# Performance work log

Hardware: AMD Instinct MI355X
Metric: run time of the kernel (lower is better)

The kernel has to match this reference:

```python
import jax, jax.numpy as jnp
import numpy as np

H = 5  # hidden size == input size

def setup_inputs() -> dict:
    key = jax.random.key(0)
    ks = jax.random.split(key, 12)
    B, T = 8192, 512
    s = 1.0 / np.sqrt(H)
    x = jax.random.normal(ks[0], (B, T, H), dtype=jnp.float32)
    # LSTM params (PyTorch layout: [4H, in], gate order i,f,g,o)
    W_ih = jax.random.uniform(ks[1], (4 * H, H), jnp.float32, -s, s)
    W_hh = jax.random.uniform(ks[2], (4 * H, H), jnp.float32, -s, s)
    b_ih = jax.random.uniform(ks[3], (4 * H,), jnp.float32, -s, s)
    b_hh = jax.random.uniform(ks[4], (4 * H,), jnp.float32, -s, s)
    # MLP head 5->32->32->5 (PyTorch Linear layout: [out, in])
    W1 = jax.random.uniform(ks[5], (32, H), jnp.float32, -s, s)
    b1 = jax.random.uniform(ks[6], (32,), jnp.float32, -s, s)
    s2 = 1.0 / np.sqrt(32)
    W2 = jax.random.uniform(ks[7], (32, 32), jnp.float32, -s2, s2)
    b2 = jax.random.uniform(ks[8], (32,), jnp.float32, -s2, s2)
    W3 = jax.random.uniform(ks[9], (H, 32), jnp.float32, -s2, s2)
    b3 = jax.random.uniform(ks[10], (H,), jnp.float32, -s2, s2)
    return {"x": x, "W_ih": W_ih, "W_hh": W_hh, "b_ih": b_ih, "b_hh": b_hh,
            "W1": W1, "b1": b1, "W2": W2, "b2": b2, "W3": W3, "b3": b3}


def _lstm_last_hidden(x, W_ih, W_hh, b_ih, b_hh):
    # x: [B, T, H]. Precompute input projections for all steps: [T, B, 4H]
    xz = jnp.einsum('bth,gh->tbg', x, W_ih) + (b_ih + b_hh)
    B = x.shape[0]
    h0 = jnp.zeros((B, H), x.dtype)
    c0 = jnp.zeros((B, H), x.dtype)

    def step(carry, z_t):
        h, c = carry
        z = z_t + h @ W_hh.T  # [B, 4H]
        i = jax.nn.sigmoid(z[:, 0:H])
        f = jax.nn.sigmoid(z[:, H:2 * H])
        g = jnp.tanh(z[:, 2 * H:3 * H])
        o = jax.nn.sigmoid(z[:, 3 * H:4 * H])
        c = f * c + i * g
        h = o * jnp.tanh(c)
        return (h, c), None

    (h, _), _ = jax.lax.scan(step, (h0, c0), xz)
    return h  # [B, H]


def reference(x, W_ih, W_hh, b_ih, b_hh, W1, b1, W2, b2, W3, b3):
    h_last = _lstm_last_hidden(x, W_ih, W_hh, b_ih, b_hh)
    out = h_last + x[:, -1, :]                # residual with last input step
    out = jax.nn.relu(out @ W1.T + b1)
    out = jax.nn.relu(out @ W2.T + b2)
    out = out @ W3.T + b3
    return out
```

## Files before the change

kernel.cpp:

```cpp
#include <hip/hip_runtime.h>


#define LOG2E 1.44269504088896f

__device__ __forceinline__ float hexp2(float x) { return __builtin_amdgcn_exp2f(x); }
__device__ __forceinline__ float hrcp(float x)  { return __builtin_amdgcn_rcpf(x); }

template<int CTRL>
__device__ __forceinline__ float dpp_mov(float x) {
  int r = __builtin_amdgcn_update_dpp(0, __builtin_bit_cast(int, x),
                                      CTRL, 0xF, 0xF, true);
  return __builtin_bit_cast(float, r);
}
template<int CTRL, int BANKMASK>
__device__ __forceinline__ float dpp_merge(float old, float src) {
  int r = __builtin_amdgcn_update_dpp(__builtin_bit_cast(int, old),
                                      __builtin_bit_cast(int, src),
                                      CTRL, 0xF, BANKMASK, false);
  return __builtin_bit_cast(float, r);
}

constexpr int TT   = 512;
constexpr int HD   = 5;
constexpr int RPB  = 8;
constexpr int CHNK = 32;
constexpr int RSTR = 164;
constexpr int XOFF = RPB * RSTR;
constexpr int NCH  = TT / CHNK;

__global__ __attribute__((amdgpu_flat_work_group_size(64, 64),
                          amdgpu_waves_per_eu(1, 1)))
void lstm_mlp_kernel(
    const float* __restrict__ x,   const float* __restrict__ Wih,
    const float* __restrict__ Whh, const float* __restrict__ bih,
    const float* __restrict__ bhh, const float* __restrict__ W1,
    const float* __restrict__ b1,  const float* __restrict__ W2,
    const float* __restrict__ b2,  const float* __restrict__ W3,
    const float* __restrict__ b3,  float* __restrict__ out, int B)
{
  const int lane = threadIdx.x;
  const int grp  = lane >> 3;
  const int j    = lane & 7;
  const int jj   = (j < 5) ? j : 0;
  const int blockRow = blockIdx.x * RPB;
  const int row  = blockRow + grp;
  const bool act = (j < 5) && (row < B);

  __shared__ __align__(16) float xbuf[2 * XOFF];
  __shared__ float s1[RPB][32];
  __shared__ float s2[RPB][32];

  float wih[4][5], whh[4][5], bsum[4];
#pragma unroll
  for (int G = 0; G < 4; ++G) {
    const float sc = (G == 2) ? (2.0f * LOG2E) : (-LOG2E);
#pragma unroll
    for (int k = 0; k < 5; ++k) {
      wih[G][k] = Wih[(G * 5 + jj) * 5 + k] * sc;
      whh[G][k] = Whh[(G * 5 + jj) * 5 + k] * sc;
    }
    bsum[G] = (bih[G * 5 + jj] + bhh[G * 5 + jj]) * sc;
  }

  const int rowc = (row < B) ? row : (B - 1);
  const float xl0 = x[(size_t)rowc * (TT * HD) + 511 * HD + 0];
  const float xl1 = x[(size_t)rowc * (TT * HD) + 511 * HD + 1];
  const float xl2 = x[(size_t)rowc * (TT * HD) + 511 * HD + 2];
  const float xl3 = x[(size_t)rowc * (TT * HD) + 511 * HD + 3];
  const float xl4 = x[(size_t)rowc * (TT * HD) + 511 * HD + 4];

  const float4* gp[5];
  int wa[5];
#pragma unroll
  for (int i = 0; i < 5; ++i) {
    int u  = i * 64 + lane;
    int r  = u / 40;
    int o4 = u - r * 40;
    int gr = blockRow + r; if (gr >= B) gr = B - 1;
    gp[i]  = (const float4*)(x + (size_t)gr * (TT * HD)) + o4;
    wa[i]  = r * RSTR + o4 * 4;
  }

  float4 st0, st1, st2, st3, st4;
  st0 = *gp[0]; gp[0] += 40; st1 = *gp[1]; gp[1] += 40;
  st2 = *gp[2]; gp[2] += 40; st3 = *gp[3]; gp[3] += 40;
  st4 = *gp[4]; gp[4] += 40;
  *(float4*)&xbuf[wa[0]] = st0; *(float4*)&xbuf[wa[1]] = st1;
  *(float4*)&xbuf[wa[2]] = st2; *(float4*)&xbuf[wa[3]] = st3;
  *(float4*)&xbuf[wa[4]] = st4;
  st0 = *gp[0]; gp[0] += 40; st1 = *gp[1]; gp[1] += 40;
  st2 = *gp[2]; gp[2] += 40; st3 = *gp[3]; gp[3] += 40;
  st4 = *gp[4]; gp[4] += 40;

  float c = 0.0f;
  float hv0 = 0.f, hv1 = 0.f, hv2 = 0.f, hv3 = 0.f, hv4 = 0.f;
  float zx0, zx1, zx2, zx3;

  {
    const float* xp = &xbuf[grp * RSTR];
    float p0 = xp[0], p1 = xp[1], p2 = xp[2], p3 = xp[3], p4 = xp[4];
    zx0 = bsum[0];
    zx0 = fmaf(p0, wih[0][0], zx0); zx0 = fmaf(p1, wih[0][1], zx0);
    zx0 = fmaf(p2, wih[0][2], zx0); zx0 = fmaf(p3, wih[0][3], zx0);
    zx0 = fmaf(p4, wih[0][4], zx0);
    zx1 = bsum[1];
    zx1 = fmaf(p0, wih[1][0], zx1); zx1 = fmaf(p1, wih[1][1], zx1);
    zx1 = fmaf(p2, wih[1][2], zx1); zx1 = fmaf(p3, wih[1][3], zx1);
    zx1 = fmaf(p4, wih[1][4], zx1);
    zx2 = bsum[2];
    zx2 = fmaf(p0, wih[2][0], zx2); zx2 = fmaf(p1, wih[2][1], zx2);
    zx2 = fmaf(p2, wih[2][2], zx2); zx2 = fmaf(p3, wih[2][3], zx2);
    zx2 = fmaf(p4, wih[2][4], zx2);
    zx3 = bsum[3];
    zx3 = fmaf(p0, wih[3][0], zx3); zx3 = fmaf(p1, wih[3][1], zx3);
    zx3 = fmaf(p2, wih[3][2], zx3); zx3 = fmaf(p3, wih[3][3], zx3);
    zx3 = fmaf(p4, wih[3][4], zx3);
  }

  auto stepP = [&](float n0, float n1, float n2, float n3, float n4) {
    float z0 = zx0, z1 = zx1, z2 = zx2, z3 = zx3;
    z0 = fmaf(hv0, whh[0][0], z0); z0 = fmaf(hv1, whh[0][1], z0);
    z0 = fmaf(hv2, whh[0][2], z0); z0 = fmaf(hv3, whh[0][3], z0);
    z0 = fmaf(hv4, whh[0][4], z0);
    z1 = fmaf(hv0, whh[1][0], z1); z1 = fmaf(hv1, whh[1][1], z1);
    z1 = fmaf(hv2, whh[1][2], z1); z1 = fmaf(hv3, whh[1][3], z1);
    z1 = fmaf(hv4, whh[1][4], z1);
    z2 = fmaf(hv0, whh[2][0], z2); z2 = fmaf(hv1, whh[2][1], z2);
    z2 = fmaf(hv2, whh[2][2], z2); z2 = fmaf(hv3, whh[2][3], z2);
    z2 = fmaf(hv4, whh[2][4], z2);
    z3 = fmaf(hv0, whh[3][0], z3); z3 = fmaf(hv1, whh[3][1], z3);
    z3 = fmaf(hv2, whh[3][2], z3); z3 = fmaf(hv3, whh[3][3], z3);
    z3 = fmaf(hv4, whh[3][4], z3);
    float e0 = hexp2(z0), e1 = hexp2(z1), e2 = hexp2(z2), e3 = hexp2(z3);
    float n_0 = bsum[0];
    n_0 = fmaf(n0, wih[0][0], n_0); n_0 = fmaf(n1, wih[0][1], n_0);
    n_0 = fmaf(n2, wih[0][2], n_0); n_0 = fmaf(n3, wih[0][3], n_0);
    n_0 = fmaf(n4, wih[0][4], n_0);
    float n_1 = bsum[1];
    n_1 = fmaf(n0, wih[1][0], n_1); n_1 = fmaf(n1, wih[1][1], n_1);
    n_1 = fmaf(n2, wih[1][2], n_1); n_1 = fmaf(n3, wih[1][3], n_1);
    n_1 = fmaf(n4, wih[1][4], n_1);
    float fg = hrcp(1.0f + e1);
    float ig = hrcp(1.0f + e0);
    float gr = hrcp(1.0f + e2);
    float og = hrcp(1.0f + e3);
    float gv = fmaf(-2.0f, gr, 1.0f);
    c = fmaf(fg, c, ig * gv);
    float cm = c * (2.0f * LOG2E);
    float ec = hexp2(cm);
    float n_2 = bsum[2];
    n_2 = fmaf(n0, wih[2][0], n_2); n_2 = fmaf(n1, wih[2][1], n_2);
    n_2 = fmaf(n2, wih[2][2], n_2); n_2 = fmaf(n3, wih[2][3], n_2);
    n_2 = fmaf(n4, wih[2][4], n_2);
    float n_3 = bsum[3];
    n_3 = fmaf(n0, wih[3][0], n_3); n_3 = fmaf(n1, wih[3][1], n_3);
    n_3 = fmaf(n2, wih[3][2], n_3); n_3 = fmaf(n3, wih[3][3], n_3);
    n_3 = fmaf(n4, wih[3][4], n_3);
    float th = fmaf(-2.0f, hrcp(1.0f + ec), 1.0f);
    float h  = og * th;
    float q0 = dpp_mov<0x00>(h);
    float q1 = dpp_mov<0x55>(h);
    float q2 = dpp_mov<0xAA>(h);
    float q3 = dpp_mov<0xFF>(h);
    hv0 = dpp_merge<0x114, 0xA>(q0, q0);
    hv1 = dpp_merge<0x114, 0xA>(q1, q1);
    hv2 = dpp_merge<0x114, 0xA>(q2, q2);
    hv3 = dpp_merge<0x114, 0xA>(q3, q3);
    hv4 = dpp_merge<0x104, 0x5>(q0, q0);
    zx0 = n_0; zx1 = n_1; zx2 = n_2; zx3 = n_3;
  };

  float4 A0, A1, A2, A3, A4;
  float4 B0, B1, B2, B3, B4;

  auto rdg = [&](int fi, float4& A, float4& Bv, float4& C, float4& D, float4& E) {
    const float4* p = (const float4*)&xbuf[fi];
    A = p[0]; Bv = p[1]; C = p[2]; D = p[3]; E = p[4];
  };

  auto SUBA = [&]() {
    stepP(A1.y, A1.z, A1.w, A2.x, A2.y);
    stepP(A2.z, A2.w, A3.x, A3.y, A3.z);
    stepP(A3.w, A4.x, A4.y, A4.z, A4.w);
    stepP(B0.x, B0.y, B0.z, B0.w, B1.x);
  };
  auto SUBB = [&]() {
    stepP(B1.y, B1.z, B1.w, B2.x, B2.y);
    stepP(B2.z, B2.w, B3.x, B3.y, B3.z);
    stepP(B3.w, B4.x, B4.y, B4.z, B4.w);
    stepP(A0.x, A0.y, A0.z, A0.w, A1.x);
  };

#pragma unroll 1
  for (int ch = 0; ch < NCH; ++ch) {
    const int bo_cur  = (ch & 1) ? XOFF : 0;
    const int bo_next = XOFF - bo_cur;
    if (ch < NCH - 1) {
      *(float4*)&xbuf[wa[0] + bo_next] = st0;
      *(float4*)&xbuf[wa[1] + bo_next] = st1;
      *(float4*)&xbuf[wa[2] + bo_next] = st2;
      *(float4*)&xbuf[wa[3] + bo_next] = st3;
      *(float4*)&xbuf[wa[4] + bo_next] = st4;
    }
    if (ch < NCH - 2) {
      st0 = *gp[0]; gp[0] += 40; st1 = *gp[1]; gp[1] += 40;
      st2 = *gp[2]; gp[2] += 40; st3 = *gp[3]; gp[3] += 40;
      st4 = *gp[4]; gp[4] += 40;
    }
    const int xb = bo_cur + grp * RSTR;
    rdg(xb +   0, A0, A1, A2, A3, A4);
    rdg(xb +  20, B0, B1, B2, B3, B4);
    SUBA(); rdg(xb +  40, A0, A1, A2, A3, A4);
    SUBB(); rdg(xb +  60, B0, B1, B2, B3, B4);
    SUBA(); rdg(xb +  80, A0, A1, A2, A3, A4);
    SUBB(); rdg(xb + 100, B0, B1, B2, B3, B4);
    SUBA(); rdg(xb + 120, A0, A1, A2, A3, A4);
    SUBB(); rdg(xb + 140, B0, B1, B2, B3, B4);
    SUBA();
    rdg(bo_next + grp * RSTR, A0, A1, A2, A3, A4);
    SUBB();
  }

  float in5_0 = hv0 + xl0, in5_1 = hv1 + xl1, in5_2 = hv2 + xl2,
        in5_3 = hv3 + xl3, in5_4 = hv4 + xl4;

#pragma unroll
  for (int p = 0; p < 4; ++p) {
    int m = p * 8 + j;
    float acc = b1[m];
    acc = fmaf(W1[m * 5 + 0], in5_0, acc);
    acc = fmaf(W1[m * 5 + 1], in5_1, acc);
    acc = fmaf(W1[m * 5 + 2], in5_2, acc);
    acc = fmaf(W1[m * 5 + 3], in5_3, acc);
    acc = fmaf(W1[m * 5 + 4], in5_4, acc);
    s1[grp][m] = fmaxf(acc, 0.0f);
  }
  float y1[32];
#pragma unroll
  for (int k = 0; k < 32; ++k) y1[k] = s1[grp][k];

  auto dot32 = [&](const float* W, int m, const float* y, float b) {
    float acc = b;
    const float4* w4 = (const float4*)(W + m * 32);
#pragma unroll
    for (int k4 = 0; k4 < 8; ++k4) {
      float4 w = w4[k4];
      acc = fmaf(w.x, y[k4 * 4 + 0], acc);
      acc = fmaf(w.y, y[k4 * 4 + 1], acc);
      acc = fmaf(w.z, y[k4 * 4 + 2], acc);
      acc = fmaf(w.w, y[k4 * 4 + 3], acc);
    }
    return acc;
  };

#pragma unroll
  for (int p = 0; p < 4; ++p) {
    int m = p * 8 + j;
    s2[grp][m] = fmaxf(dot32(W2, m, y1, b2[m]), 0.0f);
  }
  float y2[32];
#pragma unroll
  for (int k = 0; k < 32; ++k) y2[k] = s2[grp][k];

  if (act) out[row * HD + j] = dot32(W3, j, y2, b3[j]);
}

extern "C" void kernel_launch(void* const* d_in, const int* in_sizes, int n_in,
                              void* d_out, int out_size, void* d_ws, size_t ws_size,
                              hipStream_t stream) {
  const float* x   = (const float*)d_in[0];
  const float* Wih = (const float*)d_in[1];
  const float* Whh = (const float*)d_in[2];
  const float* bih = (const float*)d_in[3];
  const float* bhh = (const float*)d_in[4];
  const float* W1  = (const float*)d_in[5];
  const float* b1  = (const float*)d_in[6];
  const float* W2  = (const float*)d_in[7];
  const float* b2  = (const float*)d_in[8];
  const float* W3  = (const float*)d_in[9];
  const float* b3  = (const float*)d_in[10];

  int B = in_sizes[0] / (TT * HD);
  int grid = (B + RPB - 1) / RPB;
  hipLaunchKernelGGL(lstm_mlp_kernel, dim3(grid), dim3(64), 0, stream,
                     x, Wih, Whh, bih, bhh, W1, b1, W2, b2, W3, b3,
                     (float*)d_out, B);
}
```

Measured before the change: 204.5 us.

## Pair gate reciprocals, prefetch input projection two steps ahead, pin schedule

Gate reciprocals are combined in pairs: one rcp of (1+e0)(1+e2) and one of (1+e1)(1+e3) replace four separate rcps, and the gates are recovered with multiplies. This shortens the transcendental chain on the serial recurrence. The input projection is now computed two timesteps ahead, so the stepping offsets into the staged x buffer shift. sched_barrier calls pin how the off-critical-path projection FMAs interleave with the recurrence. The paired products can overflow if the gate exponents get large, and the gate exponent signs now rely on weights folded in elsewhere.

```diff
diff --git a/kernel.cpp b/kernel.cpp
--- a/kernel.cpp
+++ b/kernel.cpp
@@ -5,6 +5,7 @@
 
 __device__ __forceinline__ float hexp2(float x) { return __builtin_amdgcn_exp2f(x); }
 __device__ __forceinline__ float hrcp(float x)  { return __builtin_amdgcn_rcpf(x); }
+#define SBAR() __builtin_amdgcn_sched_barrier(0)
 
 template<int CTRL>
 __device__ __forceinline__ float dpp_mov(float x) {
@@ -94,31 +95,35 @@
 
   float c = 0.0f;
   float hv0 = 0.f, hv1 = 0.f, hv2 = 0.f, hv3 = 0.f, hv4 = 0.f;
-  float zx0, zx1, zx2, zx3;
+  float zxA0, zxA1, zxA2, zxA3;
+  float zxB0, zxB1, zxB2, zxB3;
 
   {
     const float* xp = &xbuf[grp * RSTR];
-    float p0 = xp[0], p1 = xp[1], p2 = xp[2], p3 = xp[3], p4 = xp[4];
-    zx0 = bsum[0];
-    zx0 = fmaf(p0, wih[0][0], zx0); zx0 = fmaf(p1, wih[0][1], zx0);
-    zx0 = fmaf(p2, wih[0][2], zx0); zx0 = fmaf(p3, wih[0][3], zx0);
-    zx0 = fmaf(p4, wih[0][4], zx0);
-    zx1 = bsum[1];
-    zx1 = fmaf(p0, wih[1][0], zx1); zx1 = fmaf(p1, wih[1][1], zx1);
-    zx1 = fmaf(p2, wih[1][2], zx1); zx1 = fmaf(p3, wih[1][3], zx1);
-    zx1 = fmaf(p4, wih[1][4], zx1);
-    zx2 = bsum[2];
-    zx2 = fmaf(p0, wih[2][0], zx2); zx2 = fmaf(p1, wih[2][1], zx2);
-    zx2 = fmaf(p2, wih[2][2], zx2); zx2 = fmaf(p3, wih[2][3], zx2);
-    zx2 = fmaf(p4, wih[2][4], zx2);
-    zx3 = bsum[3];
-    zx3 = fmaf(p0, wih[3][0], zx3); zx3 = fmaf(p1, wih[3][1], zx3);
-    zx3 = fmaf(p2, wih[3][2], zx3); zx3 = fmaf(p3, wih[3][3], zx3);
-    zx3 = fmaf(p4, wih[3][4], zx3);
+#pragma unroll
+    for (int s = 0; s < 2; ++s) {
+      float p0 = xp[5*s+0], p1 = xp[5*s+1], p2 = xp[5*s+2],
+            p3 = xp[5*s+3], p4 = xp[5*s+4];
+      float t0 = bsum[0], t1 = bsum[1], t2 = bsum[2], t3 = bsum[3];
+      t0 = fmaf(p0, wih[0][0], t0); t0 = fmaf(p1, wih[0][1], t0);
+      t0 = fmaf(p2, wih[0][2], t0); t0 = fmaf(p3, wih[0][3], t0);
+      t0 = fmaf(p4, wih[0][4], t0);
+      t1 = fmaf(p0, wih[1][0], t1); t1 = fmaf(p1, wih[1][1], t1);
+      t1 = fmaf(p2, wih[1][2], t1); t1 = fmaf(p3, wih[1][3], t1);
+      t1 = fmaf(p4, wih[1][4], t1);
+      t2 = fmaf(p0, wih[2][0], t2); t2 = fmaf(p1, wih[2][1], t2);
+      t2 = fmaf(p2, wih[2][2], t2); t2 = fmaf(p3, wih[2][3], t2);
+      t2 = fmaf(p4, wih[2][4], t2);
+      t3 = fmaf(p0, wih[3][0], t3); t3 = fmaf(p1, wih[3][1], t3);
+      t3 = fmaf(p2, wih[3][2], t3); t3 = fmaf(p3, wih[3][3], t3);
+      t3 = fmaf(p4, wih[3][4], t3);
+      if (s == 0) { zxA0 = t0; zxA1 = t1; zxA2 = t2; zxA3 = t3; }
+      else        { zxB0 = t0; zxB1 = t1; zxB2 = t2; zxB3 = t3; }
+    }
   }
 
   auto stepP = [&](float n0, float n1, float n2, float n3, float n4) {
-    float z0 = zx0, z1 = zx1, z2 = zx2, z3 = zx3;
+    float z0 = zxA0, z1 = zxA1, z2 = zxA2, z3 = zxA3;
     z0 = fmaf(hv0, whh[0][0], z0); z0 = fmaf(hv1, whh[0][1], z0);
     z0 = fmaf(hv2, whh[0][2], z0); z0 = fmaf(hv3, whh[0][3], z0);
     z0 = fmaf(hv4, whh[0][4], z0);
@@ -131,7 +136,11 @@
     z3 = fmaf(hv0, whh[3][0], z3); z3 = fmaf(hv1, whh[3][1], z3);
     z3 = fmaf(hv2, whh[3][2], z3); z3 = fmaf(hv3, whh[3][3], z3);
     z3 = fmaf(hv4, whh[3][4], z3);
-    float e0 = hexp2(z0), e1 = hexp2(z1), e2 = hexp2(z2), e3 = hexp2(z3);
+    float e2 = hexp2(z2);
+    float e0 = hexp2(z0);
+    float e1 = hexp2(z1);
+    float e3 = hexp2(z3);
+    SBAR();
     float n_0 = bsum[0];
     n_0 = fmaf(n0, wih[0][0], n_0); n_0 = fmaf(n1, wih[0][1], n_0);
     n_0 = fmaf(n2, wih[0][2], n_0); n_0 = fmaf(n3, wih[0][3], n_0);
@@ -140,24 +149,37 @@
     n_1 = fmaf(n0, wih[1][0], n_1); n_1 = fmaf(n1, wih[1][1], n_1);
     n_1 = fmaf(n2, wih[1][2], n_1); n_1 = fmaf(n3, wih[1][3], n_1);
     n_1 = fmaf(n4, wih[1][4], n_1);
-    float fg = hrcp(1.0f + e1);
-    float ig = hrcp(1.0f + e0);
-    float gr = hrcp(1.0f + e2);
-    float og = hrcp(1.0f + e3);
-    float gv = fmaf(-2.0f, gr, 1.0f);
-    c = fmaf(fg, c, ig * gv);
-    float cm = c * (2.0f * LOG2E);
-    float ec = hexp2(cm);
+    SBAR();
+    float A2 = 1.0f + e2;
+    float A0 = 1.0f + e0;
+    float m02 = A0 * A2;
+    float r02 = hrcp(m02);
+    float A1 = 1.0f + e1;
+    float A3 = 1.0f + e3;
+    float m13 = A1 * A3;
+    float r13 = hrcp(m13);
+    SBAR();
     float n_2 = bsum[2];
     n_2 = fmaf(n0, wih[2][0], n_2); n_2 = fmaf(n1, wih[2][1], n_2);
     n_2 = fmaf(n2, wih[2][2], n_2); n_2 = fmaf(n3, wih[2][3], n_2);
     n_2 = fmaf(n4, wih[2][4], n_2);
+    SBAR();
+    float t2g = A2 - 2.0f;
+    float ig  = t2g * r02;
+    float fg  = A3 * r13;
+    float og  = A1 * r13;
+    c = fmaf(fg, c, ig);
+    float ec = hexp2(c * (2.0f * LOG2E));
+    SBAR();
     float n_3 = bsum[3];
     n_3 = fmaf(n0, wih[3][0], n_3); n_3 = fmaf(n1, wih[3][1], n_3);
     n_3 = fmaf(n2, wih[3][2], n_3); n_3 = fmaf(n3, wih[3][3], n_3);
     n_3 = fmaf(n4, wih[3][4], n_3);
-    float th = fmaf(-2.0f, hrcp(1.0f + ec), 1.0f);
-    float h  = og * th;
+    float o2 = og + og;
+    SBAR();
+    float Ac = 1.0f + ec;
+    float rc = hrcp(Ac);
+    float h = fmaf(-o2, rc, og);
     float q0 = dpp_mov<0x00>(h);
     float q1 = dpp_mov<0x55>(h);
     float q2 = dpp_mov<0xAA>(h);
@@ -167,28 +189,29 @@
     hv2 = dpp_merge<0x114, 0xA>(q2, q2);
     hv3 = dpp_merge<0x114, 0xA>(q3, q3);
     hv4 = dpp_merge<0x104, 0x5>(q0, q0);
-    zx0 = n_0; zx1 = n_1; zx2 = n_2; zx3 = n_3;
-  };
-
-  float4 A0, A1, A2, A3, A4;
-  float4 B0, B1, B2, B3, B4;
-
-  auto rdg = [&](int fi, float4& A, float4& Bv, float4& C, float4& D, float4& E) {
+    zxA0 = zxB0; zxA1 = zxB1; zxA2 = zxB2; zxA3 = zxB3;
+    zxB0 = n_0;  zxB1 = n_1;  zxB2 = n_2;  zxB3 = n_3;
+  };
+
+  float4 A0v, A1v, A2v, A3v, A4v;
+  float4 B0v, B1v, B2v, B3v, B4v;
+
+  auto rdg = [&](int fi, float4& Av, float4& Bv, float4& Cv, float4& Dv, float4& Ev) {
     const float4* p = (const float4*)&xbuf[fi];
-    A = p[0]; Bv = p[1]; C = p[2]; D = p[3]; E = p[4];
+    Av = p[0]; Bv = p[1]; Cv = p[2]; Dv = p[3]; Ev = p[4];
   };
 
   auto SUBA = [&]() {
-    stepP(A1.y, A1.z, A1.w, A2.x, A2.y);
-    stepP(A2.z, A2.w, A3.x, A3.y, A3.z);
-    stepP(A3.w, A4.x, A4.y, A4.z, A4.w);
-    stepP(B0.x, B0.y, B0.z, B0.w, B1.x);
+    stepP(A2v.z, A2v.w, A3v.x, A3v.y, A3v.z);
+    stepP(A3v.w, A4v.x, A4v.y, A4v.z, A4v.w);
+    stepP(B0v.x, B0v.y, B0v.z, B0v.w, B1v.x);
+    stepP(B1v.y, B1v.z, B1v.w, B2v.x, B2v.y);
   };
   auto SUBB = [&]() {
-    stepP(B1.y, B1.z, B1.w, B2.x, B2.y);
-    stepP(B2.z, B2.w, B3.x, B3.y, B3.z);
-    stepP(B3.w, B4.x, B4.y, B4.z, B4.w);
-    stepP(A0.x, A0.y, A0.z, A0.w, A1.x);
+    stepP(B2v.z, B2v.w, B3v.x, B3v.y, B3v.z);
+    stepP(B3v.w, B4v.x, B4v.y, B4v.z, B4v.w);
+    stepP(A0v.x, A0v.y, A0v.z, A0v.w, A1v.x);
+    stepP(A1v.y, A1v.z, A1v.w, A2v.x, A2v.y);
   };
 
 #pragma unroll 1
@@ -208,16 +231,16 @@
       st4 = *gp[4]; gp[4] += 40;
     }
     const int xb = bo_cur + grp * RSTR;
-    rdg(xb +   0, A0, A1, A2, A3, A4);
-    rdg(xb +  20, B0, B1, B2, B3, B4);
-    SUBA(); rdg(xb +  40, A0, A1, A2, A3, A4);
-    SUBB(); rdg(xb +  60, B0, B1, B2, B3, B4);
-    SUBA(); rdg(xb +  80, A0, A1, A2, A3, A4);
-    SUBB(); rdg(xb + 100, B0, B1, B2, B3, B4);
-    SUBA(); rdg(xb + 120, A0, A1, A2, A3, A4);
-    SUBB(); rdg(xb + 140, B0, B1, B2, B3, B4);
+    rdg(xb +   0, A0v, A1v, A2v, A3v, A4v);
+    rdg(xb +  20, B0v, B1v, B2v, B3v, B4v);
+    SUBA(); rdg(xb +  40, A0v, A1v, A2v, A3v, A4v);
+    SUBB(); rdg(xb +  60, B0v, B1v, B2v, B3v, B4v);
+    SUBA(); rdg(xb +  80, A0v, A1v, A2v, A3v, A4v);
+    SUBB(); rdg(xb + 100, B0v, B1v, B2v, B3v, B4v);
+    SUBA(); rdg(xb + 120, A0v, A1v, A2v, A3v, A4v);
+    SUBB(); rdg(xb + 140, B0v, B1v, B2v, B3v, B4v);
     SUBA();
-    rdg(bo_next + grp * RSTR, A0, A1, A2, A3, A4);
+    rdg(bo_next + grp * RSTR, A0v, A1v, A2v, A3v, A4v);
     SUBB();
   }
 
```

After: 207.1 us. No clear change (+1.3%).
